# Performance work log

Hardware: AMD Instinct MI355X
Metric: run time of the kernel (lower is better)

The kernel has to match this reference:

```python
import jax, jax.numpy as jnp
import numpy as np

B, S, D = 2, 2048, 256
QK, H, MLP = 256, 8, 1024
TOPK, R, MD = 8, 2048, 64
HD = QK // H
SCALE = HD ** -0.5
AVG_DEG = 32.0


def _layernorm(x, g, b, eps=1e-5):
    m = jnp.mean(x, axis=-1, keepdims=True)
    v = jnp.var(x, axis=-1, keepdims=True)
    return (x - m) * jax.lax.rsqrt(v + eps) * g + b


def _neighbor_mask(adj_matrix, region_memory, region_indices):
    # cluster neighbors: cosine-sim top-k over region memory, diagonal excluded
    nrm = jnp.linalg.norm(region_memory, axis=1, keepdims=True)
    nm = region_memory / (nrm + 1e-8)
    sim = nm @ nm.T                                   # [R, R]
    sim = jnp.where(jnp.eye(R, dtype=bool), -jnp.inf, sim)
    _, idx = jax.lax.top_k(sim, TOPK)                 # [R, TOPK]
    cmask = jnp.zeros((R, R), dtype=bool).at[jnp.arange(R)[:, None], idx].set(True)
    ext = adj_matrix | cmask                          # extended neighborhood [R, R]
    # token i attends to token positions j in neighborhood(region_indices[i]), j < S
    return ext[region_indices][:, :S]                 # [S, S] bool


def setup_inputs() -> dict:
    key = jax.random.key(0)
    ks = jax.random.split(key, 24)
    sc = 0.02
    inp = {
        "x": jax.random.normal(ks[0], (B, S, D), jnp.float32),
        "region_indices": jax.random.randint(ks[1], (S,), 0, R),
        "adj_matrix": jax.random.uniform(ks[2], (R, R)) < (AVG_DEG / R),
        "region_memory": jax.random.normal(ks[3], (R, MD), jnp.float32),
        # weights stored [in, out] (torch Linear is x @ W.T + b)
        "wq": jax.random.normal(ks[4], (D, QK)) * sc, "bq": jnp.zeros((QK,)),
        "wk": jax.random.normal(ks[5], (D, QK)) * sc, "bk": jnp.zeros((QK,)),
        "wv": jax.random.normal(ks[6], (D, QK)) * sc, "bv": jnp.zeros((QK,)),
        "wo": jax.random.normal(ks[7], (QK, D)) * sc, "bo": jnp.zeros((D,)),
        "ln1_g": jnp.ones((D,)), "ln1_b": jnp.zeros((D,)),
        "ln2_g": jnp.ones((D,)), "ln2_b": jnp.zeros((D,)),
        "gate_w": jax.random.normal(ks[8], (2 * D, D)) * sc, "gate_b": jnp.zeros((D,)),
        "ffn_w1": jax.random.normal(ks[9], (D, MLP)) * sc, "ffn_b1": jnp.zeros((MLP,)),
        "ffn_w2": jax.random.normal(ks[10], (MLP, D)) * sc, "ffn_b2": jnp.zeros((D,)),
    }
    return inp


def reference(x, region_indices, adj_matrix, region_memory,
              wq, bq, wk, bk, wv, bv, wo, bo,
              ln1_g, ln1_b, ln2_g, ln2_b,
              gate_w, gate_b, ffn_w1, ffn_b1, ffn_w2, ffn_b2):
    mask = _neighbor_mask(adj_matrix, region_memory, region_indices)  # [S, S]

    xn = _layernorm(x, ln1_g, ln1_b)
    q = (xn @ wq + bq).reshape(B, S, H, HD).transpose(0, 2, 1, 3)  # b h s d
    k = (xn @ wk + bk).reshape(B, S, H, HD).transpose(0, 2, 1, 3)
    v = (xn @ wv + bv).reshape(B, S, H, HD).transpose(0, 2, 1, 3)

    dots = jnp.einsum('bhid,bhjd->bhij', q, k) * SCALE
    # faithful to source: non-neighbor scores stay 0 (NOT -inf), softmax over all j
    scores = jnp.where(mask[None, None], dots, 0.0)
    attn = jax.nn.softmax(scores, axis=-1)
    out = jnp.einsum('bhij,bhjd->bhid', attn, v)
    out = out.transpose(0, 2, 1, 3).reshape(B, S, QK)
    attn_out = out @ wo + bo

    gate = jax.nn.sigmoid(jnp.concatenate([x, attn_out], axis=-1) @ gate_w + gate_b)
    fused = gate * x + (1.0 - gate) * attn_out

    h = _layernorm(fused, ln2_g, ln2_b)
    ffn_out = jax.nn.gelu(h @ ffn_w1 + ffn_b1, approximate=False) @ ffn_w2 + ffn_b2
    return fused + ffn_out
```

## Files before the change

### kernel.cpp

```cpp
#include <hip/hip_runtime.h>
#include <hip/hip_bf16.h>
#include <math.h>

#define B_ 2
#define S_ 2048
#define D_ 256
#define QK_ 256
#define H_ 8
#define HD_ 32
#define MLP_ 1024
#define TOPK_ 8
#define R_ 2048
#define MD_ 64
#define MAXN_ 192

using bf16_t = __hip_bfloat16;
using bf16x8 = __attribute__((ext_vector_type(8))) short;
using f32x4  = __attribute__((ext_vector_type(4))) float;

__device__ __constant__ float SCALE_ = 0.17677669529663687f;

__device__ inline float bf2f(short s) {
    union { unsigned int u; float f; } cvt;
    cvt.u = ((unsigned int)(unsigned short)s) << 16;
    return cvt.f;
}

__global__ void detect_adj(const unsigned int* __restrict__ adj, int* __restrict__ flag) {
    long g = (long)blockIdx.x * blockDim.x + threadIdx.x;
    long n = (long)R_ * R_ / 4;
    int found = 0;
    for (long i = g; i < n; i += (long)gridDim.x * blockDim.x) {
        if (adj[i] > 1u) { found = 1; break; }
    }
    if (found) atomicOr(flag, 1);
}

__device__ inline bool adj_on(const void* adj, int isbyte, long idx) {
    if (isbyte) return ((const unsigned char*)adj)[idx] != 0;
    return ((const int*)adj)[idx] != 0;
}

__global__ void norm_rm(const float* __restrict__ rm, bf16_t* __restrict__ nm_bf,
                        int* __restrict__ flag) {
    int r = blockIdx.x, t = threadIdx.x;
    if (r == 0 && t == 0) *flag = 0;
    float v = rm[r * MD_ + t];
    float s = v * v;
    for (int o = 32; o > 0; o >>= 1) s += __shfl_down(s, o);
    s = __shfl(s, 0);
    nm_bf[r * MD_ + t] = __float2bfloat16(v / (sqrtf(s) + 1e-8f));
}

__global__ __launch_bounds__(256) void topk_sel(const float* __restrict__ sim,
                                                int* __restrict__ tk) {
    int t = threadIdx.x;
    int w = t >> 6, ln = t & 63;
    int r = blockIdx.x * 4 + w;
    const float4* row4 = (const float4*)(sim + (long)r * R_);
    float4 f4[8];
#pragma unroll
    for (int k = 0; k < 8; k++) f4[k] = row4[ln + 64 * k];
    {
        int rem = (r >> 2) & 63, kw = r >> 8, jw = r & 3;
        if (rem == ln) {
#pragma unroll
            for (int k = 0; k < 8; k++)
                if (k == kw) {
                    if (jw == 0) f4[k].x = -INFINITY;
                    else if (jw == 1) f4[k].y = -INFINITY;
                    else if (jw == 2) f4[k].z = -INFINITY;
                    else f4[k].w = -INFINITY;
                }
        }
    }
    for (int it = 0; it < TOPK_; it++) {
        float bv = -INFINITY; int bi = 0x7fffffff;
#pragma unroll
        for (int k = 0; k < 8; k++) {
            int c0 = 4 * (ln + 64 * k);
            if (f4[k].x > bv) { bv = f4[k].x; bi = c0; }
            if (f4[k].y > bv) { bv = f4[k].y; bi = c0 + 1; }
            if (f4[k].z > bv) { bv = f4[k].z; bi = c0 + 2; }
            if (f4[k].w > bv) { bv = f4[k].w; bi = c0 + 3; }
        }
#pragma unroll
        for (int o = 32; o > 0; o >>= 1) {
            float ov = __shfl_down(bv, o); int oi = __shfl_down(bi, o);
            if (ov > bv || (ov == bv && oi < bi)) { bv = ov; bi = oi; }
        }
        int xi = __shfl(bi, 0);
        if (ln == 0) tk[r * TOPK_ + it] = xi;
        int rem = (xi >> 2) & 63, kw = xi >> 8, jw = xi & 3;
        if (rem == ln) {
#pragma unroll
            for (int k = 0; k < 8; k++)
                if (k == kw) {
                    if (jw == 0) f4[k].x = -INFINITY;
                    else if (jw == 1) f4[k].y = -INFINITY;
                    else if (jw == 2) f4[k].z = -INFINITY;
                    else f4[k].w = -INFINITY;
                }
        }
    }
}

__global__ __launch_bounds__(256) void build_nbr(const void* __restrict__ adj,
                                                 const int* __restrict__ tk,
                                                 const int* __restrict__ flag,
                                                 int* __restrict__ nbr_idx,
                                                 int* __restrict__ nbr_cnt) {
    __shared__ int cnt;
    int r = blockIdx.x, t = threadIdx.x;
    if (t == 0) cnt = 0;
    __syncthreads();
    int isbyte = *flag;
    for (int c = t; c < S_; c += 256) {
        long idx = (long)r * R_ + c;
        if (adj_on(adj, isbyte, idx)) {
            int p = atomicAdd(&cnt, 1);
            if (p < MAXN_) nbr_idx[r * MAXN_ + p] = c;
        }
    }
    __syncthreads();
    if (t < TOPK_) {
        int c = tk[r * TOPK_ + t];
        long idx = (long)r * R_ + c;
        if (!adj_on(adj, isbyte, idx) && c < S_) {
            int p = atomicAdd(&cnt, 1);
            if (p < MAXN_) nbr_idx[r * MAXN_ + p] = c;
        }
    }
    __syncthreads();
    if (t == 0) nbr_cnt[r] = min(cnt, MAXN_);
}

__global__ __launch_bounds__(256) void ln_kernel(const float* __restrict__ x,
                                                 const float* __restrict__ g,
                                                 const float* __restrict__ b,
                                                 bf16_t* __restrict__ y,
                                                 bf16_t* __restrict__ xcat) {
    __shared__ float red[256];
    int row = blockIdx.x, t = threadIdx.x;
    float v = x[(long)row * D_ + t];
    xcat[(long)row * 512 + t] = __float2bfloat16(v);
    red[t] = v; __syncthreads();
    for (int o = 128; o > 0; o >>= 1) { if (t < o) red[t] += red[t + o]; __syncthreads(); }
    float mean = red[0] / D_;
    __syncthreads();
    float dv = v - mean;
    red[t] = dv * dv; __syncthreads();
    for (int o = 128; o > 0; o >>= 1) { if (t < o) red[t] += red[t + o]; __syncthreads(); }
    float var = red[0] / D_;
    y[(long)row * D_ + t] = __float2bfloat16(dv * rsqrtf(var + 1e-5f) * g[t] + b[t]);
}

__global__ __launch_bounds__(256) void conv_w(const float* w0, const float* w1, const float* w2,
                                              const float* w3, const float* w4, const float* w5,
                                              const float* w6,
                                              const float* bq, const float* bk, const float* bv,
                                              bf16_t* wt, float* bqkv) {
    __shared__ float tile[32][33];
    int tb = blockIdx.x;
    if (tb >= 896) {
        int t = (tb - 896) * 256 + threadIdx.x;
        if (t < 768) bqkv[t] = t < 256 ? bq[t] : (t < 512 ? bk[t - 256] : bv[t - 512]);
        return;
    }
    const float* W; long dstoff; int K, N, local;
    if (tb < 64)       { W = w0; dstoff = 0;       K = 256;  N = 256;  local = tb; }
    else if (tb < 128) { W = w1; dstoff = 65536;   K = 256;  N = 256;  local = tb - 64; }
    else if (tb < 192) { W = w2; dstoff = 131072;  K = 256;  N = 256;  local = tb - 128; }
    else if (tb < 256) { W = w3; dstoff = 196608;  K = 256;  N = 256;  local = tb - 192; }
    else if (tb < 384) { W = w4; dstoff = 262144;  K = 512;  N = 256;  local = tb - 256; }
    else if (tb < 640) { W = w5; dstoff = 393216;  K = 256;  N = 1024; local = tb - 384; }
    else               { W = w6; dstoff = 655360;  K = 1024; N = 256;  local = tb - 640; }
    int ntn = N >> 5;
    int tk = local / ntn, tn = local - tk * ntn;
    int k0 = tk * 32, n0 = tn * 32;
    int r = threadIdx.x >> 5, c = threadIdx.x & 31;
#pragma unroll
    for (int rr = 0; rr < 4; rr++)
        tile[r + rr * 8][c] = W[(long)(k0 + r + rr * 8) * N + n0 + c];
    __syncthreads();
    bf16_t* dst = wt + dstoff;
#pragma unroll
    for (int rr = 0; rr < 4; rr++)
        dst[(long)(n0 + r + rr * 8) * K + k0 + c] = __float2bfloat16(tile[c][r + rr * 8]);
}

#define LDT64 72

template<int GELU>
__global__ __launch_bounds__(256) void mgemm64(const bf16_t* __restrict__ A,
                                               const bf16_t* __restrict__ Wt,
                                               const float* __restrict__ bias,
                                               const float* __restrict__ resid,
                                               float* __restrict__ Cf,
                                               bf16_t* __restrict__ Cb,
                                               int M, int N, int K, int ldcb) {
    __shared__ short As[64 * LDT64];
    __shared__ short Bs[64 * LDT64];
    int tid = threadIdx.x;
    int m0 = blockIdx.y * 64, n0 = blockIdx.x * 64;
    int w = tid >> 6, ln = tid & 63;
    int wr = w >> 1, wc = w & 1;
    int srow = tid >> 2, skb = (tid & 3) * 8;
    f32x4 zero4 = {0.f, 0.f, 0.f, 0.f};
    f32x4 acc[2][2];
#pragma unroll
    for (int i = 0; i < 2; i++)
#pragma unroll
        for (int j = 0; j < 2; j++) acc[i][j] = zero4;

    const bf16_t* Ab = A + (long)m0 * K + skb;
    const bf16_t* Bb = Wt + (long)n0 * K + skb;

    for (int k0 = 0; k0 < K; k0 += 64) {
        uint4 a0 = *(const uint4*)(Ab + (long)srow * K + k0);
        uint4 a1 = *(const uint4*)(Ab + (long)srow * K + k0 + 32);
        uint4 b0 = *(const uint4*)(Bb + (long)srow * K + k0);
        uint4 b1 = *(const uint4*)(Bb + (long)srow * K + k0 + 32);
        *(uint4*)(&As[srow * LDT64 + skb]) = a0;
        *(uint4*)(&As[srow * LDT64 + skb + 32]) = a1;
        *(uint4*)(&Bs[srow * LDT64 + skb]) = b0;
        *(uint4*)(&Bs[srow * LDT64 + skb + 32]) = b1;
        __syncthreads();
        int kr = (ln >> 4) * 8;
        int arow = wr * 32 + (ln & 15);
        int brow = wc * 32 + (ln & 15);
        bf16x8 af[2][2], bfr[2][2];
#pragma unroll
        for (int mi = 0; mi < 2; mi++)
#pragma unroll
            for (int ks = 0; ks < 2; ks++)
                af[mi][ks] = *(const bf16x8*)(&As[(arow + mi * 16) * LDT64 + ks * 32 + kr]);
#pragma unroll
        for (int ni = 0; ni < 2; ni++)
#pragma unroll
            for (int ks = 0; ks < 2; ks++)
                bfr[ni][ks] = *(const bf16x8*)(&Bs[(brow + ni * 16) * LDT64 + ks * 32 + kr]);
#pragma unroll
        for (int mi = 0; mi < 2; mi++)
#pragma unroll
            for (int ni = 0; ni < 2; ni++) {
                acc[mi][ni] = __builtin_amdgcn_mfma_f32_16x16x32_bf16(af[mi][0], bfr[ni][0], acc[mi][ni], 0, 0, 0);
                acc[mi][ni] = __builtin_amdgcn_mfma_f32_16x16x32_bf16(af[mi][1], bfr[ni][1], acc[mi][ni], 0, 0, 0);
            }
        __syncthreads();
    }
    int colb = n0 + wc * 32 + (ln & 15);
    int rowb = m0 + wr * 32 + (ln >> 4) * 4;
#pragma unroll
    for (int ni = 0; ni < 2; ni++) {
        int col = colb + ni * 16;
        float bv = bias ? bias[col] : 0.f;
#pragma unroll
        for (int mi = 0; mi < 2; mi++) {
#pragma unroll
            for (int r = 0; r < 4; r++) {
                int row = rowb + mi * 16 + r;
                float v = acc[mi][ni][r] + bv;
                if (GELU) v = 0.5f * v * (1.0f + erff(v * 0.70710678118654752f));
                if (resid) v += resid[(long)row * N + col];
                if (Cf) Cf[(long)row * N + col] = v;
                if (Cb) Cb[(long)row * ldcb + col] = __float2bfloat16(v);
            }
        }
    }
}

__global__ void vsum1(const bf16_t* __restrict__ qkv, float* __restrict__ part) {
    int b = blockIdx.x >> 6, ch = blockIdx.x & 63;
    int c = threadIdx.x;
    float s = 0.f;
    int j0 = ch * 32;
    for (int j = j0; j < j0 + 32; j++)
        s += __bfloat162float(qkv[((long)b * S_ + j) * 768 + 512 + c]);
    part[(long)blockIdx.x * QK_ + c] = s;
}

__global__ void vsum2(const float* __restrict__ part, float* __restrict__ vs) {
    int g = blockIdx.x * 256 + threadIdx.x;
    int b = g >> 8, c = g & 255;
    float s = 0.f;
    for (int ch = 0; ch < 64; ch++) s += part[(long)(b * 64 + ch) * QK_ + c];
    vs[g] = s;
}

__global__ __launch_bounds__(256) void attn_kernel(const bf16_t* __restrict__ qkv,
                                                   const float* __restrict__ vs,
                                                   const int* __restrict__ ridx,
                                                   const int* __restrict__ nbr_idx,
                                                   const int* __restrict__ nbr_cnt,
                                                   bf16_t* __restrict__ out) {
    __shared__ float qs[QK_];
    __shared__ float ej[H_][MAXN_];
    __shared__ int   nb[MAXN_];
    int bi = blockIdx.x;
    int b = bi >> 11, i = bi & (S_ - 1);
    int t = threadIdx.x;
    int h = t >> 5, ln = t & 31;
    int r = ridx[i];
    int cnt = nbr_cnt[r];
    qs[t] = __bfloat162float(qkv[(long)bi * 768 + t]);
    for (int p = t; p < cnt; p += 256) nb[p] = nbr_idx[r * MAXN_ + p];
    __syncthreads();
    const bf16_t* kvb = qkv + (long)b * S_ * 768;
    int quad = ln & 3, pslot = ln >> 2;
    const float* qh = qs + h * HD_;
    float qreg[8];
#pragma unroll
    for (int e = 0; e < 8; e++) qreg[e] = qh[quad * 8 + e];
    float lmax = 0.0f;
#pragma unroll 2
    for (int s = 0; s * 8 < cnt; s++) {
        int p = s * 8 + pslot;
        float sc = 0.f;
        if (p < cnt) {
            int j = nb[p];
            bf16x8 kk = *(const bf16x8*)(kvb + (long)j * 768 + 256 + h * HD_ + quad * 8);
#pragma unroll
            for (int e = 0; e < 8; e++) sc = fmaf(qreg[e], bf2f(kk[e]), sc);
        }
        sc += __shfl_xor(sc, 1, 32);
        sc += __shfl_xor(sc, 2, 32);
        sc *= SCALE_;
        if (p < cnt) {
            if (quad == 0) ej[h][p] = sc;
            lmax = fmaxf(lmax, sc);
        }
    }
#pragma unroll
    for (int o = 16; o > 0; o >>= 1) lmax = fmaxf(lmax, __shfl_xor(lmax, o, 32));
    float lz = 0.f;
#pragma unroll
    for (int u = 0; u < 6; u++) {
        int p = ln + 32 * u;
        if (p < cnt) {
            float e = expf(ej[h][p] - lmax);
            ej[h][p] = e;
            lz += e;
        }
    }
#pragma unroll
    for (int o = 16; o > 0; o >>= 1) lz += __shfl_xor(lz, o, 32);
    float em = expf(-lmax);
    float Z = lz + (float)(S_ - cnt) * em;
    float accv = 0.f, vn = 0.f;
    const bf16_t* vbase = kvb + 512 + h * HD_ + ln;
#pragma unroll 8
    for (int p = 0; p < cnt; p++) {
        int j = nb[p];
        float vv = __bfloat162float(vbase[(long)j * 768]);
        float e = ej[h][p];
        accv = fmaf(e, vv, accv);
        vn += vv;
    }
    float o = (em * (vs[b * QK_ + h * HD_ + ln] - vn) + accv) / Z;
    out[(long)bi * QK_ + h * HD_ + ln] = __float2bfloat16(o);
}

__global__ __launch_bounds__(256) void fuse_ln2_kernel(const float* __restrict__ x,
                                                       const float* __restrict__ ao,
                                                       const float* __restrict__ gp,
                                                       const float* __restrict__ g2,
                                                       const float* __restrict__ b2,
                                                       float* __restrict__ fused,
                                                       bf16_t* __restrict__ h) {
    __shared__ float red[256];
    int row = blockIdx.x, t = threadIdx.x;
    long idx = (long)row * D_ + t;
    float gate = 1.f / (1.f + expf(-gp[idx]));
    float f = gate * x[idx] + (1.f - gate) * ao[idx];
    fused[idx] = f;
    red[t] = f; __syncthreads();
    for (int o = 128; o > 0; o >>= 1) { if (t < o) red[t] += red[t + o]; __syncthreads(); }
    float mean = red[0] / D_;
    __syncthreads();
    float dv = f - mean;
    red[t] = dv * dv; __syncthreads();
    for (int o = 128; o > 0; o >>= 1) { if (t < o) red[t] += red[t + o]; __syncthreads(); }
    float var = red[0] / D_;
    h[idx] = __float2bfloat16(dv * rsqrtf(var + 1e-5f) * g2[t] + b2[t]);
}

extern "C" void kernel_launch(void* const* d_in, const int* in_sizes, int n_in,
                              void* d_out, int out_size, void* d_ws, size_t ws_size,
                              hipStream_t stream) {
    const float* x    = (const float*)d_in[0];
    const int*   ridx = (const int*)d_in[1];
    const void*  adj  = d_in[2];
    const float* rm   = (const float*)d_in[3];
    const float* wq = (const float*)d_in[4],  *bq = (const float*)d_in[5];
    const float* wk = (const float*)d_in[6],  *bk = (const float*)d_in[7];
    const float* wv = (const float*)d_in[8],  *bv = (const float*)d_in[9];
    const float* wo = (const float*)d_in[10], *bo = (const float*)d_in[11];
    const float* ln1g = (const float*)d_in[12], *ln1b = (const float*)d_in[13];
    const float* ln2g = (const float*)d_in[14], *ln2b = (const float*)d_in[15];
    const float* gw  = (const float*)d_in[16], *gb  = (const float*)d_in[17];
    const float* fw1 = (const float*)d_in[18], *fb1 = (const float*)d_in[19];
    const float* fw2 = (const float*)d_in[20], *fb2 = (const float*)d_in[21];
    float* out = (float*)d_out;

    float* wsf      = (float*)d_ws;
    int*   flag     = (int*)d_ws;
    bf16_t* nm_bf   = (bf16_t*)(wsf + 64);
    int*   tk       = (int*)(wsf + 64 + 131072);
    int*   nbr_idx  = tk + 16384;
    int*   nbr_cnt  = nbr_idx + R_ * MAXN_;
    bf16_t* qkv_bf  = (bf16_t*)(nbr_cnt + 2048);
    float* vs       = (float*)(nbr_cnt + 2048) + 3145728;
    float* gatep    = vs + 512;
    float* attn_out = gatep + 1048576;
    float* fusedb   = attn_out + 1048576;
    float* part     = fusedb + 1048576;
    bf16_t* xn_bf   = (bf16_t*)(part + 32768);
    bf16_t* attnO_bf= (bf16_t*)((float*)xn_bf + 524288);
    bf16_t* xcat_bf = (bf16_t*)((float*)attnO_bf + 524288);
    bf16_t* hb_bf   = (bf16_t*)((float*)xcat_bf + 1048576);
    bf16_t* f1_bf   = (bf16_t*)((float*)hb_bf + 524288);
    bf16_t* WT      = (bf16_t*)((float*)f1_bf + 2097152);
    float* bqkv     = (float*)WT + 458752;
    float* sim      = bqkv + 768;

    const int MROWS = B_ * S_;

    norm_rm<<<R_, 64, 0, stream>>>(rm, nm_bf, flag);
    detect_adj<<<256, 256, 0, stream>>>((const unsigned int*)adj, flag);

    mgemm64<0><<<dim3(R_ / 64, R_ / 64), 256, 0, stream>>>(
        nm_bf, nm_bf, nullptr, nullptr, sim, nullptr, R_, R_, MD_, 0);
    topk_sel<<<R_ / 4, 256, 0, stream>>>(sim, tk);

    build_nbr<<<R_, 256, 0, stream>>>(adj, tk, flag, nbr_idx, nbr_cnt);

    conv_w<<<899, 256, 0, stream>>>(wq, wk, wv, wo, gw, fw1, fw2, bq, bk, bv, WT, bqkv);

    ln_kernel<<<MROWS, 256, 0, stream>>>(x, ln1g, ln1b, xn_bf, xcat_bf);

    mgemm64<0><<<dim3(768 / 64, MROWS / 64), 256, 0, stream>>>(
        xn_bf, WT + 0, bqkv, nullptr, nullptr, qkv_bf, MROWS, 768, 256, 768);

    vsum1<<<B_ * 64, 256, 0, stream>>>(qkv_bf, part);
    vsum2<<<2, 256, 0, stream>>>(part, vs);
    attn_kernel<<<MROWS, 256, 0, stream>>>(qkv_bf, vs, ridx, nbr_idx, nbr_cnt, attnO_bf);

    mgemm64<0><<<dim3(256 / 64, MROWS / 64), 256, 0, stream>>>(
        attnO_bf, WT + 196608, bo, nullptr, attn_out, xcat_bf + 256, MROWS, 256, 256, 512);

    mgemm64<0><<<dim3(256 / 64, MROWS / 64), 256, 0, stream>>>(
        xcat_bf, WT + 262144, gb, nullptr, gatep, nullptr, MROWS, 256, 512, 0);

    fuse_ln2_kernel<<<MROWS, 256, 0, stream>>>(x, attn_out, gatep, ln2g, ln2b, fusedb, hb_bf);

    mgemm64<1><<<dim3(1024 / 64, MROWS / 64), 256, 0, stream>>>(
        hb_bf, WT + 393216, fb1, nullptr, nullptr, f1_bf, MROWS, 1024, 256, 1024);

    mgemm64<0><<<dim3(256 / 64, MROWS / 64), 256, 0, stream>>>(
        f1_bf, WT + 655360, fb2, fusedb, out, nullptr, MROWS, 256, 1024, 0);
}
```

Measured before the change: 132.2 us.

## Fold output projection into gate GEMM, split-K FFN2 with atomics, warp-level layernorms

Precomputes Wo·Wg_attn so the attention output projection and the gate pre-activation come out of one N=512 GEMM. The x-part of the gate is computed in a separate GEMM that overlaps with attention preparation, and its result is added as a residual. The fused/LN2 kernel now writes fused+b2 straight into the output, and FFN2 runs split-K over two slices that atomically add into the output. The layernorm kernels switch to wave-shuffle reductions with float4 loads at four rows per block. This removes a launch and intermediate traffic, at the cost of extra weight-preprocessing GEMMs, float atomics with nondeterministic summation order, and an extra bf16 rounding of the combined weight.

```diff
diff --git a/kernel.cpp b/kernel.cpp
--- a/kernel.cpp
+++ b/kernel.cpp
@@ -24,6 +24,11 @@
     union { unsigned int u; float f; } cvt;
     cvt.u = ((unsigned int)(unsigned short)s) << 16;
     return cvt.f;
+}
+__device__ inline short f2bfs(float f) {
+    union { bf16_t b; short s; } u;
+    u.b = __float2bfloat16(f);
+    return u.s;
 }
 
 __global__ void detect_adj(const unsigned int* __restrict__ adj, int* __restrict__ flag) {
@@ -138,67 +143,88 @@
 __global__ __launch_bounds__(256) void ln_kernel(const float* __restrict__ x,
                                                  const float* __restrict__ g,
                                                  const float* __restrict__ b,
-                                                 bf16_t* __restrict__ y,
-                                                 bf16_t* __restrict__ xcat) {
-    __shared__ float red[256];
-    int row = blockIdx.x, t = threadIdx.x;
-    float v = x[(long)row * D_ + t];
-    xcat[(long)row * 512 + t] = __float2bfloat16(v);
-    red[t] = v; __syncthreads();
-    for (int o = 128; o > 0; o >>= 1) { if (t < o) red[t] += red[t + o]; __syncthreads(); }
-    float mean = red[0] / D_;
-    __syncthreads();
-    float dv = v - mean;
-    red[t] = dv * dv; __syncthreads();
-    for (int o = 128; o > 0; o >>= 1) { if (t < o) red[t] += red[t + o]; __syncthreads(); }
-    float var = red[0] / D_;
-    y[(long)row * D_ + t] = __float2bfloat16(dv * rsqrtf(var + 1e-5f) * g[t] + b[t]);
+                                                 bf16_t* __restrict__ xn_bf,
+                                                 bf16_t* __restrict__ x_bf) {
+    int t = threadIdx.x;
+    int row = blockIdx.x * 4 + (t >> 6), ln = t & 63, c = ln * 4;
+    float4 v4 = *(const float4*)(x + (long)row * D_ + c);
+    *(short4*)(x_bf + (long)row * D_ + c) =
+        make_short4(f2bfs(v4.x), f2bfs(v4.y), f2bfs(v4.z), f2bfs(v4.w));
+    float s = v4.x + v4.y + v4.z + v4.w;
+#pragma unroll
+    for (int o = 32; o > 0; o >>= 1) s += __shfl_xor(s, o);
+    float mean = s * (1.f / D_);
+    float d0 = v4.x - mean, d1 = v4.y - mean, d2 = v4.z - mean, d3 = v4.w - mean;
+    float q = d0 * d0 + d1 * d1 + d2 * d2 + d3 * d3;
+#pragma unroll
+    for (int o = 32; o > 0; o >>= 1) q += __shfl_xor(q, o);
+    float rs = rsqrtf(q * (1.f / D_) + 1e-5f);
+    float4 g4 = *(const float4*)(g + c);
+    float4 b4 = *(const float4*)(b + c);
+    *(short4*)(xn_bf + (long)row * D_ + c) =
+        make_short4(f2bfs(d0 * rs * g4.x + b4.x), f2bfs(d1 * rs * g4.y + b4.y),
+                    f2bfs(d2 * rs * g4.z + b4.z), f2bfs(d3 * rs * g4.w + b4.w));
 }
 
 __global__ __launch_bounds__(256) void conv_w(const float* w0, const float* w1, const float* w2,
                                               const float* w3, const float* w4, const float* w5,
                                               const float* w6,
                                               const float* bq, const float* bk, const float* bv,
-                                              bf16_t* wt, float* bqkv) {
+                                              const float* bo, const float* gb,
+                                              bf16_t* wt, bf16_t* WB, bf16_t* wo_nt,
+                                              float* bqkv, float* bb) {
     __shared__ float tile[32][33];
-    int tb = blockIdx.x;
+    int tb = blockIdx.x, t = threadIdx.x;
+    if (tb >= 963) {
+        float s = gb[t];
+        for (int o = 0; o < 256; o++) s += bo[o] * w4[(long)(256 + o) * 256 + t];
+        bb[t] = bo[t];
+        bb[256 + t] = s;
+        return;
+    }
+    if (tb >= 899) {
+        long idx = (long)(tb - 899) * 1024 + t * 4;
+        float4 v = *(const float4*)(w3 + idx);
+        *(short4*)(wo_nt + idx) = make_short4(f2bfs(v.x), f2bfs(v.y), f2bfs(v.z), f2bfs(v.w));
+        return;
+    }
     if (tb >= 896) {
-        int t = (tb - 896) * 256 + threadIdx.x;
-        if (t < 768) bqkv[t] = t < 256 ? bq[t] : (t < 512 ? bk[t - 256] : bv[t - 512]);
+        int tt = (tb - 896) * 256 + t;
+        if (tt < 768) bqkv[tt] = tt < 256 ? bq[tt] : (tt < 512 ? bk[tt - 256] : bv[tt - 512]);
         return;
     }
-    const float* W; long dstoff; int K, N, local;
-    if (tb < 64)       { W = w0; dstoff = 0;       K = 256;  N = 256;  local = tb; }
-    else if (tb < 128) { W = w1; dstoff = 65536;   K = 256;  N = 256;  local = tb - 64; }
-    else if (tb < 192) { W = w2; dstoff = 131072;  K = 256;  N = 256;  local = tb - 128; }
-    else if (tb < 256) { W = w3; dstoff = 196608;  K = 256;  N = 256;  local = tb - 192; }
-    else if (tb < 384) { W = w4; dstoff = 262144;  K = 512;  N = 256;  local = tb - 256; }
-    else if (tb < 640) { W = w5; dstoff = 393216;  K = 256;  N = 1024; local = tb - 384; }
-    else               { W = w6; dstoff = 655360;  K = 1024; N = 256;  local = tb - 640; }
+    const float* W; bf16_t* dst; long dstoff; int K, N, local;
+    if (tb < 64)       { W = w0; dst = wt; dstoff = 0;       K = 256;  N = 256;  local = tb; }
+    else if (tb < 128) { W = w1; dst = wt; dstoff = 65536;   K = 256;  N = 256;  local = tb - 64; }
+    else if (tb < 192) { W = w2; dst = wt; dstoff = 131072;  K = 256;  N = 256;  local = tb - 128; }
+    else if (tb < 256) { W = w3; dst = WB; dstoff = 0;       K = 256;  N = 256;  local = tb - 192; }
+    else if (tb < 384) { W = w4; dst = wt; dstoff = 262144;  K = 512;  N = 256;  local = tb - 256; }
+    else if (tb < 640) { W = w5; dst = wt; dstoff = 393216;  K = 256;  N = 1024; local = tb - 384; }
+    else               { W = w6; dst = wt; dstoff = 655360;  K = 1024; N = 256;  local = tb - 640; }
     int ntn = N >> 5;
-    int tk = local / ntn, tn = local - tk * ntn;
-    int k0 = tk * 32, n0 = tn * 32;
-    int r = threadIdx.x >> 5, c = threadIdx.x & 31;
+    int tk2 = local / ntn, tn = local - tk2 * ntn;
+    int k0 = tk2 * 32, n0 = tn * 32;
+    int r = t >> 5, c = t & 31;
 #pragma unroll
     for (int rr = 0; rr < 4; rr++)
         tile[r + rr * 8][c] = W[(long)(k0 + r + rr * 8) * N + n0 + c];
     __syncthreads();
-    bf16_t* dst = wt + dstoff;
+    bf16_t* d2 = dst + dstoff;
 #pragma unroll
     for (int rr = 0; rr < 4; rr++)
-        dst[(long)(n0 + r + rr * 8) * K + k0 + c] = __float2bfloat16(tile[c][r + rr * 8]);
+        d2[(long)(n0 + r + rr * 8) * K + k0 + c] = __float2bfloat16(tile[c][r + rr * 8]);
 }
 
 #define LDT64 72
 
-template<int GELU>
-__global__ __launch_bounds__(256) void mgemm64(const bf16_t* __restrict__ A,
-                                               const bf16_t* __restrict__ Wt,
+template<int GELU, int CTRANS, int RESH, int ATOMIC>
+__global__ __launch_bounds__(256) void mgemm64(const bf16_t* __restrict__ A, int lda,
+                                               const bf16_t* __restrict__ Bt, int ldb,
                                                const float* __restrict__ bias,
-                                               const float* __restrict__ resid,
-                                               float* __restrict__ Cf,
-                                               bf16_t* __restrict__ Cb,
-                                               int M, int N, int K, int ldcb) {
+                                               const float* __restrict__ resid, int ldres,
+                                               float* __restrict__ Cf, int ldcf,
+                                               bf16_t* __restrict__ Cb, int ldcb,
+                                               int N, int K) {
     __shared__ short As[64 * LDT64];
     __shared__ short Bs[64 * LDT64];
     int tid = threadIdx.x;
@@ -213,14 +239,15 @@
 #pragma unroll
         for (int j = 0; j < 2; j++) acc[i][j] = zero4;
 
-    const bf16_t* Ab = A + (long)m0 * K + skb;
-    const bf16_t* Bb = Wt + (long)n0 * K + skb;
-
-    for (int k0 = 0; k0 < K; k0 += 64) {
-        uint4 a0 = *(const uint4*)(Ab + (long)srow * K + k0);
-        uint4 a1 = *(const uint4*)(Ab + (long)srow * K + k0 + 32);
-        uint4 b0 = *(const uint4*)(Bb + (long)srow * K + k0);
-        uint4 b1 = *(const uint4*)(Bb + (long)srow * K + k0 + 32);
+    const bf16_t* Ab = A + (long)m0 * lda + skb;
+    const bf16_t* Bb = Bt + (long)n0 * ldb + skb;
+    int kbeg = ATOMIC ? blockIdx.z * K : 0;
+
+    for (int k0 = kbeg; k0 < kbeg + K; k0 += 64) {
+        uint4 a0 = *(const uint4*)(Ab + (long)srow * lda + k0);
+        uint4 a1 = *(const uint4*)(Ab + (long)srow * lda + k0 + 32);
+        uint4 b0 = *(const uint4*)(Bb + (long)srow * ldb + k0);
+        uint4 b1 = *(const uint4*)(Bb + (long)srow * ldb + k0 + 32);
         *(uint4*)(&As[srow * LDT64 + skb]) = a0;
         *(uint4*)(&As[srow * LDT64 + skb + 32]) = a1;
         *(uint4*)(&Bs[srow * LDT64 + skb]) = b0;
@@ -262,9 +289,14 @@
                 int row = rowb + mi * 16 + r;
                 float v = acc[mi][ni][r] + bv;
                 if (GELU) v = 0.5f * v * (1.0f + erff(v * 0.70710678118654752f));
-                if (resid) v += resid[(long)row * N + col];
-                if (Cf) Cf[(long)row * N + col] = v;
-                if (Cb) Cb[(long)row * ldcb + col] = __float2bfloat16(v);
+                if (RESH) { if (col >= 256) v += resid[(long)row * ldres + col - 256]; }
+                else if (resid) v += resid[(long)row * ldres + col];
+                if (ATOMIC) atomicAdd(&Cf[(long)row * ldcf + col], v);
+                else if (Cf) Cf[(long)row * ldcf + col] = v;
+                if (Cb) {
+                    if (CTRANS) Cb[(long)col * ldcb + row] = __float2bfloat16(v);
+                    else Cb[(long)row * ldcb + col] = __float2bfloat16(v);
+                }
             }
         }
     }
@@ -362,27 +394,40 @@
 }
 
 __global__ __launch_bounds__(256) void fuse_ln2_kernel(const float* __restrict__ x,
-                                                       const float* __restrict__ ao,
-                                                       const float* __restrict__ gp,
+                                                       const float* __restrict__ aog,
                                                        const float* __restrict__ g2,
                                                        const float* __restrict__ b2,
-                                                       float* __restrict__ fused,
-                                                       bf16_t* __restrict__ h) {
-    __shared__ float red[256];
-    int row = blockIdx.x, t = threadIdx.x;
-    long idx = (long)row * D_ + t;
-    float gate = 1.f / (1.f + expf(-gp[idx]));
-    float f = gate * x[idx] + (1.f - gate) * ao[idx];
-    fused[idx] = f;
-    red[t] = f; __syncthreads();
-    for (int o = 128; o > 0; o >>= 1) { if (t < o) red[t] += red[t + o]; __syncthreads(); }
-    float mean = red[0] / D_;
-    __syncthreads();
-    float dv = f - mean;
-    red[t] = dv * dv; __syncthreads();
-    for (int o = 128; o > 0; o >>= 1) { if (t < o) red[t] += red[t + o]; __syncthreads(); }
-    float var = red[0] / D_;
-    h[idx] = __float2bfloat16(dv * rsqrtf(var + 1e-5f) * g2[t] + b2[t]);
+                                                       const float* __restrict__ fb2,
+                                                       float* __restrict__ out,
+                                                       bf16_t* __restrict__ hb) {
+    int t = threadIdx.x;
+    int row = blockIdx.x * 4 + (t >> 6), ln = t & 63, c = ln * 4;
+    float4 ao4 = *(const float4*)(aog + (long)row * 512 + c);
+    float4 gp4 = *(const float4*)(aog + (long)row * 512 + 256 + c);
+    float4 x4  = *(const float4*)(x + (long)row * D_ + c);
+    float g0 = 1.f / (1.f + expf(-gp4.x)), g1 = 1.f / (1.f + expf(-gp4.y));
+    float g2v = 1.f / (1.f + expf(-gp4.z)), g3 = 1.f / (1.f + expf(-gp4.w));
+    float f0 = g0 * x4.x + (1.f - g0) * ao4.x;
+    float f1 = g1 * x4.y + (1.f - g1) * ao4.y;
+    float f2 = g2v * x4.z + (1.f - g2v) * ao4.z;
+    float f3 = g3 * x4.w + (1.f - g3) * ao4.w;
+    float4 fb4 = *(const float4*)(fb2 + c);
+    float4 o4 = {f0 + fb4.x, f1 + fb4.y, f2 + fb4.z, f3 + fb4.w};
+    *(float4*)(out + (long)row * D_ + c) = o4;
+    float s = f0 + f1 + f2 + f3;
+#pragma unroll
+    for (int o = 32; o > 0; o >>= 1) s += __shfl_xor(s, o);
+    float mean = s * (1.f / D_);
+    float d0 = f0 - mean, d1 = f1 - mean, d2 = f2 - mean, d3 = f3 - mean;
+    float q = d0 * d0 + d1 * d1 + d2 * d2 + d3 * d3;
+#pragma unroll
+    for (int o = 32; o > 0; o >>= 1) q += __shfl_xor(q, o);
+    float rs = rsqrtf(q * (1.f / D_) + 1e-5f);
+    float4 gg = *(const float4*)(g2 + c);
+    float4 bb4 = *(const float4*)(b2 + c);
+    *(short4*)(hb + (long)row * D_ + c) =
+        make_short4(f2bfs(d0 * rs * gg.x + bb4.x), f2bfs(d1 * rs * gg.y + bb4.y),
+                    f2bfs(d2 * rs * gg.z + bb4.z), f2bfs(d3 * rs * gg.w + bb4.w));
 }
 
 extern "C" void kernel_launch(void* const* d_in, const int* in_sizes, int n_in,
@@ -406,57 +451,63 @@
     float* wsf      = (float*)d_ws;
     int*   flag     = (int*)d_ws;
     bf16_t* nm_bf   = (bf16_t*)(wsf + 64);
-    int*   tk       = (int*)(wsf + 64 + 131072);
+    int*   tk       = (int*)(wsf + 131136);
     int*   nbr_idx  = tk + 16384;
     int*   nbr_cnt  = nbr_idx + R_ * MAXN_;
     bf16_t* qkv_bf  = (bf16_t*)(nbr_cnt + 2048);
     float* vs       = (float*)(nbr_cnt + 2048) + 3145728;
-    float* gatep    = vs + 512;
-    float* attn_out = gatep + 1048576;
-    float* fusedb   = attn_out + 1048576;
-    float* part     = fusedb + 1048576;
+    float* aog      = vs + 512;
+    float* xg       = aog + 2097152;
+    float* part     = xg + 1048576;
     bf16_t* xn_bf   = (bf16_t*)(part + 32768);
     bf16_t* attnO_bf= (bf16_t*)((float*)xn_bf + 524288);
-    bf16_t* xcat_bf = (bf16_t*)((float*)attnO_bf + 524288);
-    bf16_t* hb_bf   = (bf16_t*)((float*)xcat_bf + 1048576);
+    bf16_t* x_bf    = (bf16_t*)((float*)attnO_bf + 524288);
+    bf16_t* hb_bf   = (bf16_t*)((float*)x_bf + 524288);
     bf16_t* f1_bf   = (bf16_t*)((float*)hb_bf + 524288);
     bf16_t* WT      = (bf16_t*)((float*)f1_bf + 2097152);
     float* bqkv     = (float*)WT + 458752;
-    float* sim      = bqkv + 768;
+    bf16_t* WB      = (bf16_t*)(bqkv + 768);
+    bf16_t* wo_nt   = (bf16_t*)((float*)WB + 65536);
+    float* bb       = (float*)wo_nt + 32768;
+    float* sim      = bb + 512;
 
     const int MROWS = B_ * S_;
 
     norm_rm<<<R_, 64, 0, stream>>>(rm, nm_bf, flag);
     detect_adj<<<256, 256, 0, stream>>>((const unsigned int*)adj, flag);
 
-    mgemm64<0><<<dim3(R_ / 64, R_ / 64), 256, 0, stream>>>(
-        nm_bf, nm_bf, nullptr, nullptr, sim, nullptr, R_, R_, MD_, 0);
+    conv_w<<<964, 256, 0, stream>>>(wq, wk, wv, wo, gw, fw1, fw2,
+                                    bq, bk, bv, bo, gb, WT, WB, wo_nt, bqkv, bb);
+
+    mgemm64<0, 1, 0, 0><<<dim3(4, 4), 256, 0, stream>>>(
+        wo_nt, 256, WT + 262144 + 256, 512, nullptr, nullptr, 0,
+        nullptr, 0, WB + 65536, 256, 256, 256);
+
+    mgemm64<0, 0, 0, 0><<<dim3(R_ / 64, R_ / 64), 256, 0, stream>>>(
+        nm_bf, 64, nm_bf, 64, nullptr, nullptr, 0, sim, 2048, nullptr, 0, R_, MD_);
     topk_sel<<<R_ / 4, 256, 0, stream>>>(sim, tk);
-
     build_nbr<<<R_, 256, 0, stream>>>(adj, tk, flag, nbr_idx, nbr_cnt);
 
-    conv_w<<<899, 256, 0, stream>>>(wq, wk, wv, wo, gw, fw1, fw2, bq, bk, bv, WT, bqkv);
-
-    ln_kernel<<<MROWS, 256, 0, stream>>>(x, ln1g, ln1b, xn_bf, xcat_bf);
-
-    mgemm64<0><<<dim3(768 / 64, MROWS / 64), 256, 0, stream>>>(
-        xn_bf, WT + 0, bqkv, nullptr, nullptr, qkv_bf, MROWS, 768, 256, 768);
+    ln_kernel<<<MROWS / 4, 256, 0, stream>>>(x, ln1g, ln1b, xn_bf, x_bf);
+
+    mgemm64<0, 0, 0, 0><<<dim3(768 / 64, MROWS / 64), 256, 0, stream>>>(
+        xn_bf, 256, WT, 256, bqkv, nullptr, 0, nullptr, 0, qkv_bf, 768, 768, 256);
+
+    mgemm64<0, 0, 0, 0><<<dim3(256 / 64, MROWS / 64), 256, 0, stream>>>(
+        x_bf, 256, WT + 262144, 512, nullptr, nullptr, 0, xg, 256, nullptr, 0, 256, 256);
 
     vsum1<<<B_ * 64, 256, 0, stream>>>(qkv_bf, part);
     vsum2<<<2, 256, 0, stream>>>(part, vs);
     attn_kernel<<<MROWS, 256, 0, stream>>>(qkv_bf, vs, ridx, nbr_idx, nbr_cnt, attnO_bf);
 
-    mgemm64<0><<<dim3(256 / 64, MROWS / 64), 256, 0, stream>>>(
-        attnO_bf, WT + 196608, bo, nullptr, attn_out, xcat_bf + 256, MROWS, 256, 256, 512);
-
-    mgemm64<0><<<dim3(256 / 64, MROWS / 64), 256, 0, stream>>>(
-        xcat_bf, WT + 262144, gb, nullptr, gatep, nullptr, MROWS, 256, 512, 0);
-
-    fuse_ln2_kernel<<<MROWS, 256, 0, stream>>>(x, attn_out, gatep, ln2g, ln2b, fusedb, hb_bf);
-
-    mgemm64<1><<<dim3(1024 / 64, MROWS / 64), 256, 0, stream>>>(
-        hb_bf, WT + 393216, fb1, nullptr, nullptr, f1_bf, MROWS, 1024, 256, 1024);
-
-    mgemm64<0><<<dim3(256 / 64, MROWS / 64), 256, 0, stream>>>(
-        f1_bf, WT + 655360, fb2, fusedb, out, nullptr, MROWS, 256, 1024, 0);
-}
+    mgemm64<0, 0, 1, 0><<<dim3(512 / 64, MROWS / 64), 256, 0, stream>>>(
+        attnO_bf, 256, WB, 256, bb, xg, 256, aog, 512, nullptr, 0, 512, 256);
+
+    fuse_ln2_kernel<<<MROWS / 4, 256, 0, stream>>>(x, aog, ln2g, ln2b, fb2, out, hb_bf);
+
+    mgemm64<1, 0, 0, 0><<<dim3(1024 / 64, MROWS / 64), 256, 0, stream>>>(
+        hb_bf, 256, WT + 393216, 256, fb1, nullptr, 0, nullptr, 0, f1_bf, 1024, 1024, 256);
+
+    mgemm64<0, 0, 0, 1><<<dim3(256 / 64, MROWS / 64, 2), 256, 0, stream>>>(
+        f1_bf, 1024, WT + 655360, 1024, nullptr, nullptr, 0, out, 256, nullptr, 0, 256, 512);
+}
```

After: 137.1 us. 3.7% more time.

## Fold V column sums, adjacency detection, and split-K atomics into existing kernels

Applied to the files above, without the earlier changes.

The global detect_adj pass is removed. Each build_nbr block now checks its own adjacency row to decide whether the matrix is byte or int. The V column sum moves into the QKV GEMM epilogue through atomics, replacing the two vsum kernels. The gate and FFN2 GEMMs become split-K with atomicAdd into outputs that are pre-initialised with biases and the residual (gate bias in ln_kernel, fused+fb2 in fuse_ln2). This removes several launches and raises parallelism for the small-N GEMMs, at the cost of nondeterministic float atomics and a per-row dtype heuristic that could misclassify rows.

```diff
diff --git a/kernel.cpp b/kernel.cpp
--- a/kernel.cpp
+++ b/kernel.cpp
@@ -26,25 +26,13 @@
     return cvt.f;
 }
 
-__global__ void detect_adj(const unsigned int* __restrict__ adj, int* __restrict__ flag) {
-    long g = (long)blockIdx.x * blockDim.x + threadIdx.x;
-    long n = (long)R_ * R_ / 4;
-    int found = 0;
-    for (long i = g; i < n; i += (long)gridDim.x * blockDim.x) {
-        if (adj[i] > 1u) { found = 1; break; }
-    }
-    if (found) atomicOr(flag, 1);
-}
-
 __device__ inline bool adj_on(const void* adj, int isbyte, long idx) {
     if (isbyte) return ((const unsigned char*)adj)[idx] != 0;
     return ((const int*)adj)[idx] != 0;
 }
 
-__global__ void norm_rm(const float* __restrict__ rm, bf16_t* __restrict__ nm_bf,
-                        int* __restrict__ flag) {
+__global__ void norm_rm(const float* __restrict__ rm, bf16_t* __restrict__ nm_bf) {
     int r = blockIdx.x, t = threadIdx.x;
-    if (r == 0 && t == 0) *flag = 0;
     float v = rm[r * MD_ + t];
     float s = v * v;
     for (int o = 32; o > 0; o >>= 1) s += __shfl_down(s, o);
@@ -107,14 +95,21 @@
 
 __global__ __launch_bounds__(256) void build_nbr(const void* __restrict__ adj,
                                                  const int* __restrict__ tk,
-                                                 const int* __restrict__ flag,
                                                  int* __restrict__ nbr_idx,
                                                  int* __restrict__ nbr_cnt) {
-    __shared__ int cnt;
+    __shared__ int cnt, bflag;
     int r = blockIdx.x, t = threadIdx.x;
-    if (t == 0) cnt = 0;
-    __syncthreads();
-    int isbyte = *flag;
+    if (t == 0) { cnt = 0; bflag = 0; }
+    __syncthreads();
+    {
+        const unsigned int* rw = (const unsigned int*)adj + (long)r * 512;
+        int found = 0;
+        for (int i = t; i < 512; i += 256)
+            if (rw[i] > 1u) found = 1;
+        if (found) atomicOr(&bflag, 1);
+    }
+    __syncthreads();
+    int isbyte = bflag;
     for (int c = t; c < S_; c += 256) {
         long idx = (long)r * R_ + c;
         if (adj_on(adj, isbyte, idx)) {
@@ -138,12 +133,15 @@
 __global__ __launch_bounds__(256) void ln_kernel(const float* __restrict__ x,
                                                  const float* __restrict__ g,
                                                  const float* __restrict__ b,
+                                                 const float* __restrict__ gb,
                                                  bf16_t* __restrict__ y,
-                                                 bf16_t* __restrict__ xcat) {
+                                                 bf16_t* __restrict__ xcat,
+                                                 float* __restrict__ gatep) {
     __shared__ float red[256];
     int row = blockIdx.x, t = threadIdx.x;
     float v = x[(long)row * D_ + t];
     xcat[(long)row * 512 + t] = __float2bfloat16(v);
+    gatep[(long)row * D_ + t] = gb[t];
     red[t] = v; __syncthreads();
     for (int o = 128; o > 0; o >>= 1) { if (t < o) red[t] += red[t + o]; __syncthreads(); }
     float mean = red[0] / D_;
@@ -159,12 +157,16 @@
                                               const float* w3, const float* w4, const float* w5,
                                               const float* w6,
                                               const float* bq, const float* bk, const float* bv,
-                                              bf16_t* wt, float* bqkv) {
+                                              bf16_t* wt, float* bqkv, float* vs) {
     __shared__ float tile[32][33];
-    int tb = blockIdx.x;
+    int tb = blockIdx.x, t = threadIdx.x;
+    if (tb == 899) {
+        vs[t] = 0.f; vs[t + 256] = 0.f;
+        return;
+    }
     if (tb >= 896) {
-        int t = (tb - 896) * 256 + threadIdx.x;
-        if (t < 768) bqkv[t] = t < 256 ? bq[t] : (t < 512 ? bk[t - 256] : bv[t - 512]);
+        int tt = (tb - 896) * 256 + t;
+        if (tt < 768) bqkv[tt] = tt < 256 ? bq[tt] : (tt < 512 ? bk[tt - 256] : bv[tt - 512]);
         return;
     }
     const float* W; long dstoff; int K, N, local;
@@ -176,9 +178,9 @@
     else if (tb < 640) { W = w5; dstoff = 393216;  K = 256;  N = 1024; local = tb - 384; }
     else               { W = w6; dstoff = 655360;  K = 1024; N = 256;  local = tb - 640; }
     int ntn = N >> 5;
-    int tk = local / ntn, tn = local - tk * ntn;
-    int k0 = tk * 32, n0 = tn * 32;
-    int r = threadIdx.x >> 5, c = threadIdx.x & 31;
+    int tk2 = local / ntn, tn = local - tk2 * ntn;
+    int k0 = tk2 * 32, n0 = tn * 32;
+    int r = t >> 5, c = t & 31;
 #pragma unroll
     for (int rr = 0; rr < 4; rr++)
         tile[r + rr * 8][c] = W[(long)(k0 + r + rr * 8) * N + n0 + c];
@@ -191,14 +193,13 @@
 
 #define LDT64 72
 
-template<int GELU>
-__global__ __launch_bounds__(256) void mgemm64(const bf16_t* __restrict__ A,
-                                               const bf16_t* __restrict__ Wt,
+template<int GELU, int ATOMIC>
+__global__ __launch_bounds__(256) void mgemm64(const bf16_t* __restrict__ A, int lda,
+                                               const bf16_t* __restrict__ Bt, int ldb,
                                                const float* __restrict__ bias,
-                                               const float* __restrict__ resid,
-                                               float* __restrict__ Cf,
-                                               bf16_t* __restrict__ Cb,
-                                               int M, int N, int K, int ldcb) {
+                                               float* __restrict__ Cf, int ldcf,
+                                               bf16_t* __restrict__ Cb, int ldcb,
+                                               float* __restrict__ vsat, int K) {
     __shared__ short As[64 * LDT64];
     __shared__ short Bs[64 * LDT64];
     int tid = threadIdx.x;
@@ -213,14 +214,15 @@
 #pragma unroll
         for (int j = 0; j < 2; j++) acc[i][j] = zero4;
 
-    const bf16_t* Ab = A + (long)m0 * K + skb;
-    const bf16_t* Bb = Wt + (long)n0 * K + skb;
-
-    for (int k0 = 0; k0 < K; k0 += 64) {
-        uint4 a0 = *(const uint4*)(Ab + (long)srow * K + k0);
-        uint4 a1 = *(const uint4*)(Ab + (long)srow * K + k0 + 32);
-        uint4 b0 = *(const uint4*)(Bb + (long)srow * K + k0);
-        uint4 b1 = *(const uint4*)(Bb + (long)srow * K + k0 + 32);
+    const bf16_t* Ab = A + (long)m0 * lda + skb;
+    const bf16_t* Bb = Bt + (long)n0 * ldb + skb;
+    int kbeg = ATOMIC ? blockIdx.z * K : 0;
+
+    for (int k0 = kbeg; k0 < kbeg + K; k0 += 64) {
+        uint4 a0 = *(const uint4*)(Ab + (long)srow * lda + k0);
+        uint4 a1 = *(const uint4*)(Ab + (long)srow * lda + k0 + 32);
+        uint4 b0 = *(const uint4*)(Bb + (long)srow * ldb + k0);
+        uint4 b1 = *(const uint4*)(Bb + (long)srow * ldb + k0 + 32);
         *(uint4*)(&As[srow * LDT64 + skb]) = a0;
         *(uint4*)(&As[srow * LDT64 + skb + 32]) = a1;
         *(uint4*)(&Bs[srow * LDT64 + skb]) = b0;
@@ -255,6 +257,7 @@
     for (int ni = 0; ni < 2; ni++) {
         int col = colb + ni * 16;
         float bv = bias ? bias[col] : 0.f;
+        float vcol = 0.f;
 #pragma unroll
         for (int mi = 0; mi < 2; mi++) {
 #pragma unroll
@@ -262,30 +265,15 @@
                 int row = rowb + mi * 16 + r;
                 float v = acc[mi][ni][r] + bv;
                 if (GELU) v = 0.5f * v * (1.0f + erff(v * 0.70710678118654752f));
-                if (resid) v += resid[(long)row * N + col];
-                if (Cf) Cf[(long)row * N + col] = v;
+                if (ATOMIC) atomicAdd(&Cf[(long)row * ldcf + col], v);
+                else if (Cf) Cf[(long)row * ldcf + col] = v;
                 if (Cb) Cb[(long)row * ldcb + col] = __float2bfloat16(v);
+                vcol += v;
             }
         }
-    }
-}
-
-__global__ void vsum1(const bf16_t* __restrict__ qkv, float* __restrict__ part) {
-    int b = blockIdx.x >> 6, ch = blockIdx.x & 63;
-    int c = threadIdx.x;
-    float s = 0.f;
-    int j0 = ch * 32;
-    for (int j = j0; j < j0 + 32; j++)
-        s += __bfloat162float(qkv[((long)b * S_ + j) * 768 + 512 + c]);
-    part[(long)blockIdx.x * QK_ + c] = s;
-}
-
-__global__ void vsum2(const float* __restrict__ part, float* __restrict__ vs) {
-    int g = blockIdx.x * 256 + threadIdx.x;
-    int b = g >> 8, c = g & 255;
-    float s = 0.f;
-    for (int ch = 0; ch < 64; ch++) s += part[(long)(b * 64 + ch) * QK_ + c];
-    vs[g] = s;
+        if (vsat && col >= 512)
+            atomicAdd(&vsat[((m0 >> 11) << 8) + (col - 512)], vcol);
+    }
 }
 
 __global__ __launch_bounds__(256) void attn_kernel(const bf16_t* __restrict__ qkv,
@@ -366,14 +354,15 @@
                                                        const float* __restrict__ gp,
                                                        const float* __restrict__ g2,
                                                        const float* __restrict__ b2,
-                                                       float* __restrict__ fused,
+                                                       const float* __restrict__ fb2,
+                                                       float* __restrict__ out,
                                                        bf16_t* __restrict__ h) {
     __shared__ float red[256];
     int row = blockIdx.x, t = threadIdx.x;
     long idx = (long)row * D_ + t;
     float gate = 1.f / (1.f + expf(-gp[idx]));
     float f = gate * x[idx] + (1.f - gate) * ao[idx];
-    fused[idx] = f;
+    out[idx] = f + fb2[t];
     red[t] = f; __syncthreads();
     for (int o = 128; o > 0; o >>= 1) { if (t < o) red[t] += red[t + o]; __syncthreads(); }
     float mean = red[0] / D_;
@@ -404,9 +393,8 @@
     float* out = (float*)d_out;
 
     float* wsf      = (float*)d_ws;
-    int*   flag     = (int*)d_ws;
     bf16_t* nm_bf   = (bf16_t*)(wsf + 64);
-    int*   tk       = (int*)(wsf + 64 + 131072);
+    int*   tk       = (int*)(wsf + 131136);
     int*   nbr_idx  = tk + 16384;
     int*   nbr_cnt  = nbr_idx + R_ * MAXN_;
     bf16_t* qkv_bf  = (bf16_t*)(nbr_cnt + 2048);
@@ -426,37 +414,33 @@
 
     const int MROWS = B_ * S_;
 
-    norm_rm<<<R_, 64, 0, stream>>>(rm, nm_bf, flag);
-    detect_adj<<<256, 256, 0, stream>>>((const unsigned int*)adj, flag);
-
-    mgemm64<0><<<dim3(R_ / 64, R_ / 64), 256, 0, stream>>>(
-        nm_bf, nm_bf, nullptr, nullptr, sim, nullptr, R_, R_, MD_, 0);
+    norm_rm<<<R_, 64, 0, stream>>>(rm, nm_bf);
+
+    mgemm64<0, 0><<<dim3(R_ / 64, R_ / 64), 256, 0, stream>>>(
+        nm_bf, 64, nm_bf, 64, nullptr, sim, 2048, nullptr, 0, nullptr, MD_);
     topk_sel<<<R_ / 4, 256, 0, stream>>>(sim, tk);
-
-    build_nbr<<<R_, 256, 0, stream>>>(adj, tk, flag, nbr_idx, nbr_cnt);
-
-    conv_w<<<899, 256, 0, stream>>>(wq, wk, wv, wo, gw, fw1, fw2, bq, bk, bv, WT, bqkv);
-
-    ln_kernel<<<MROWS, 256, 0, stream>>>(x, ln1g, ln1b, xn_bf, xcat_bf);
-
-    mgemm64<0><<<dim3(768 / 64, MROWS / 64), 256, 0, stream>>>(
-        xn_bf, WT + 0, bqkv, nullptr, nullptr, qkv_bf, MROWS, 768, 256, 768);
-
-    vsum1<<<B_ * 64, 256, 0, stream>>>(qkv_bf, part);
-    vsum2<<<2, 256, 0, stream>>>(part, vs);
+    build_nbr<<<R_, 256, 0, stream>>>(adj, tk, nbr_idx, nbr_cnt);
+
+    conv_w<<<900, 256, 0, stream>>>(wq, wk, wv, wo, gw, fw1, fw2, bq, bk, bv, WT, bqkv, vs);
+
+    ln_kernel<<<MROWS, 256, 0, stream>>>(x, ln1g, ln1b, gb, xn_bf, xcat_bf, gatep);
+
+    mgemm64<0, 0><<<dim3(768 / 64, MROWS / 64), 256, 0, stream>>>(
+        xn_bf, 256, WT, 256, bqkv, nullptr, 0, qkv_bf, 768, vs, 256);
+
     attn_kernel<<<MROWS, 256, 0, stream>>>(qkv_bf, vs, ridx, nbr_idx, nbr_cnt, attnO_bf);
 
-    mgemm64<0><<<dim3(256 / 64, MROWS / 64), 256, 0, stream>>>(
-        attnO_bf, WT + 196608, bo, nullptr, attn_out, xcat_bf + 256, MROWS, 256, 256, 512);
-
-    mgemm64<0><<<dim3(256 / 64, MROWS / 64), 256, 0, stream>>>(
-        xcat_bf, WT + 262144, gb, nullptr, gatep, nullptr, MROWS, 256, 512, 0);
-
-    fuse_ln2_kernel<<<MROWS, 256, 0, stream>>>(x, attn_out, gatep, ln2g, ln2b, fusedb, hb_bf);
-
-    mgemm64<1><<<dim3(1024 / 64, MROWS / 64), 256, 0, stream>>>(
-        hb_bf, WT + 393216, fb1, nullptr, nullptr, f1_bf, MROWS, 1024, 256, 1024);
-
-    mgemm64<0><<<dim3(256 / 64, MROWS / 64), 256, 0, stream>>>(
-        f1_bf, WT + 655360, fb2, fusedb, out, nullptr, MROWS, 256, 1024, 0);
-}
+    mgemm64<0, 0><<<dim3(256 / 64, MROWS / 64), 256, 0, stream>>>(
+        attnO_bf, 256, WT + 196608, 256, bo, attn_out, 256, xcat_bf + 256, 512, nullptr, 256);
+
+    mgemm64<0, 1><<<dim3(256 / 64, MROWS / 64, 2), 256, 0, stream>>>(
+        xcat_bf, 512, WT + 262144, 512, nullptr, gatep, 256, nullptr, 0, nullptr, 256);
+
+    fuse_ln2_kernel<<<MROWS, 256, 0, stream>>>(x, attn_out, gatep, ln2g, ln2b, fb2, out, hb_bf);
+
+    mgemm64<1, 0><<<dim3(1024 / 64, MROWS / 64), 256, 0, stream>>>(
+        hb_bf, 256, WT + 393216, 256, fb1, nullptr, 0, f1_bf, 1024, nullptr, 256);
+
+    mgemm64<0, 1><<<dim3(256 / 64, MROWS / 64, 2), 256, 0, stream>>>(
+        f1_bf, 1024, WT + 655360, 1024, nullptr, out, 256, nullptr, 0, nullptr, 512);
+}
```

After: 139.5 us. 5.6% more time.
